# Kernel optimization log

Measured on AMD Instinct MI355X. Metric: run time of the kernel, lower is better.

Reference implementation:

```python
import jax, jax.numpy as jnp
import numpy as np

NUM_LAYERS = 32
NUM_SLOTS = 128
HIDDEN = 4096
T_WRITE = 128   # == NUM_SLOTS so slot_ids form a permutation (deterministic scatter)
T_READ = 8192
EMA_ALPHA = 0.1


def setup_inputs() -> dict:
    key = jax.random.key(0)
    ks = jax.random.split(key, 4)
    values = jax.random.normal(ks[0], (T_WRITE, HIDDEN), jnp.float32)
    queries = jax.random.normal(ks[1], (T_READ, HIDDEN), jnp.float32)
    memory = jax.random.normal(ks[2], (NUM_LAYERS, NUM_SLOTS, HIDDEN), jnp.float32) * 0.02
    gate_w = jax.random.normal(ks[3], (NUM_LAYERS, HIDDEN), jnp.float32) * (1.0 / np.sqrt(HIDDEN))
    gate_b = jnp.zeros((NUM_LAYERS,), jnp.float32)
    return {
        "values": values,
        "queries": queries,
        "memory": memory,
        "gate_w": gate_w,
        "gate_b": gate_b,
        "layer_idx": 0,
        "k": 8,
        "ptr": 0,
    }


def reference(values, queries, memory, gate_w, gate_b, layer_idx, k, ptr):
    # ---- write(): EMA scatter into one layer's slots ----
    mem_l = memory[layer_idx]                                  # [N, d]
    g = jax.nn.sigmoid(values @ gate_w[layer_idx] + gate_b[layer_idx])[:, None]  # [T,1]
    T = values.shape[0]
    slot_ids = (ptr + jnp.arange(T)) % NUM_SLOTS               # [T]
    current = mem_l[slot_ids]                                  # gather [T, d]
    updated = EMA_ALPHA * g * values + (1.0 - EMA_ALPHA) * current
    mem_new = mem_l.at[slot_ids].set(updated)                  # scatter-write [N, d]

    # ---- read(): matmul -> top-k -> gather -> softmax -> weighted sum ----
    scale = 1.0 / jnp.sqrt(jnp.float32(HIDDEN))
    scores = (queries @ mem_new.T) * scale                     # [T_read, N]
    topk_scores, topk_idx = jax.lax.top_k(scores, k)           # [T_read, k]
    attn = jax.nn.softmax(topk_scores, axis=-1)                # [T_read, k]
    topk_v = mem_new[topk_idx]                                 # gather [T_read, k, d]
    out = jnp.einsum('tk,tkd->td', attn, topk_v)               # [T_read, d]
    return out
```

## Files before the change

### kernel.cpp

```cpp
#include <hip/hip_runtime.h>
#include <math.h>

#define D 4096
#define NSLOTS 128
#define TR 8192
#define NKQ 8
#define KCH 512
#define EPS_TRIG 1e-3f
#define WIN 5e-4f

typedef __attribute__((ext_vector_type(8))) short bf16x8;
typedef __attribute__((ext_vector_type(4))) float f32x4;

union BV { bf16x8 v; unsigned u[4]; };

__device__ __forceinline__ unsigned short bfrne(float x) {
  unsigned u = __float_as_uint(x);
  unsigned r = u + 0x7fffu + ((u >> 16) & 1u);
  return (unsigned short)(r >> 16);
}

__device__ __forceinline__ void gload16(const void* gsrc, void* ldst) {
  __builtin_amdgcn_global_load_lds(
      (const __attribute__((address_space(1))) void*)gsrc,
      (__attribute__((address_space(3))) void*)ldst, 16, 0, 0);
}

__global__ __launch_bounds__(256) void update_mem_kernel(
    const float* __restrict__ values, const float* __restrict__ memory,
    const float* __restrict__ gate_w, const float* __restrict__ gate_b,
    const int* __restrict__ layer_idx_p, const int* __restrict__ ptr_p,
    int T_W, float* __restrict__ ws_mem,
    unsigned short* __restrict__ MFh,
    unsigned short* __restrict__ BTFh, unsigned short* __restrict__ BTFm) {
  const int l = layer_idx_p[0], p = ptr_p[0], s = blockIdx.x, tid = threadIdx.x;
  int t0 = ((s - p) % NSLOTS + NSLOTS) % NSLOTS;
  const bool written = (t0 < T_W);
  const int t = written ? (t0 + ((T_W - 1 - t0) / NSLOTS) * NSLOTS) : 0;
  const float* mrow = memory + ((size_t)l * NSLOTS + s) * D;
  const float* vrow = values + (size_t)t * D;

  float acoef = 0.f, bcoef = 1.0f;
  if (written) {
    const float* gw = gate_w + (size_t)l * D;
    double acc = 0.0;
    for (int j = tid; j < D; j += 256)
      acc += (double)vrow[j] * (double)gw[j];
    for (int off = 32; off; off >>= 1) acc += __shfl_down(acc, off, 64);
    __shared__ double wsum[4];
    if ((tid & 63) == 0) wsum[tid >> 6] = acc;
    __syncthreads();
    double dot = wsum[0] + wsum[1] + wsum[2] + wsum[3];
    float x = (float)dot + gate_b[l];
    float g = 1.0f / (1.0f + expf(-x));
    acoef = 0.1f * g; bcoef = 0.9f;
  }

  const int sg = s >> 4, fr_s = s & 15;
  const int ksS = s >> 5, foS = (s >> 3) & 3, posS = s & 7;
  for (int j8 = tid; j8 < D / 8; j8 += 256) {
    float4 mv0 = ((const float4*)mrow)[j8 * 2];
    float4 mv1 = ((const float4*)mrow)[j8 * 2 + 1];
    float4 vv0 = make_float4(0.f, 0.f, 0.f, 0.f), vv1 = vv0;
    if (written) {
      vv0 = ((const float4*)vrow)[j8 * 2];
      vv1 = ((const float4*)vrow)[j8 * 2 + 1];
    }
    float ov[8];
    ov[0] = acoef * vv0.x + bcoef * mv0.x;
    ov[1] = acoef * vv0.y + bcoef * mv0.y;
    ov[2] = acoef * vv0.z + bcoef * mv0.z;
    ov[3] = acoef * vv0.w + bcoef * mv0.w;
    ov[4] = acoef * vv1.x + bcoef * mv1.x;
    ov[5] = acoef * vv1.y + bcoef * mv1.y;
    ov[6] = acoef * vv1.z + bcoef * mv1.z;
    ov[7] = acoef * vv1.w + bcoef * mv1.w;
    ((float4*)(ws_mem + (size_t)s * D))[j8 * 2] =
        make_float4(ov[0], ov[1], ov[2], ov[3]);
    ((float4*)(ws_mem + (size_t)s * D))[j8 * 2 + 1] =
        make_float4(ov[4], ov[5], ov[6], ov[7]);

    unsigned short h[8], md[8];
#pragma unroll
    for (int e = 0; e < 8; ++e) {
      h[e] = bfrne(ov[e]);
      float f = __uint_as_float((unsigned)h[e] << 16);
      md[e] = bfrne(ov[e] - f);
    }
    const int ks = j8 >> 2, fo = j8 & 3;
    const size_t unit = (size_t)ks * 512 + sg * 64 + fo * 16 + fr_s;
    uint4 hp;
    hp.x = (unsigned)h[0] | ((unsigned)h[1] << 16);
    hp.y = (unsigned)h[2] | ((unsigned)h[3] << 16);
    hp.z = (unsigned)h[4] | ((unsigned)h[5] << 16);
    hp.w = (unsigned)h[6] | ((unsigned)h[7] << 16);
    ((uint4*)MFh)[unit] = hp;
#pragma unroll
    for (int e = 0; e < 8; ++e) {
      int c = j8 * 8 + e;
      size_t u = ((size_t)(c >> 4) * 4 + ksS) * 64 + foS * 16 + (c & 15);
      BTFh[u * 8 + posS] = h[e];
      BTFm[u * 8 + posS] = md[e];
    }
  }
}

__global__ __launch_bounds__(256) void scores_kernel(
    const float* __restrict__ queries, const unsigned short* __restrict__ MFh,
    float* __restrict__ part) {
  __shared__ float Qs[2][4096];

  const int tid = threadIdx.x, lane = tid & 63, w = tid >> 6;
  const int fr = lane & 15, fo = lane >> 4;
  const int qt = blockIdx.x >> 3, kq = blockIdx.x & (NKQ - 1);
  const int qbase = qt * 128;
  const int kbase = kq * KCH;

  const int rl = lane >> 3, ul = lane & 7;
  const int su = ul ^ rl;
  const float* qsrc[4];
#pragma unroll
  for (int i = 0; i < 4; ++i) {
    int g = w * 4 + i;
    qsrc[i] = queries + (size_t)(qbase + 8 * g + rl) * D + kbase + su * 4;
  }

  const unsigned short* bh_base = MFh + (size_t)lane * 8;
  const size_t kqoff = (size_t)kq * 16 * 512 * 8;

  f32x4 acc[2][8];
#pragma unroll
  for (int rg = 0; rg < 2; ++rg)
#pragma unroll
    for (int cg = 0; cg < 8; ++cg) acc[rg][cg] = (f32x4){0.f, 0.f, 0.f, 0.f};

#define STG(B, S) do {                                                       \
    const int k0_ = (S) * 32;                                                \
    _Pragma("unroll")                                                        \
    for (int i = 0; i < 4; ++i)                                              \
      gload16(qsrc[i] + k0_, &Qs[B][(w * 4 + i) * 256]);                     \
  } while (0)

#define CMP(B, S) do {                                                       \
    const size_t soff = kqoff + (size_t)(S) * 512 * 8;                       \
    bf16x8 bh_[8];                                                           \
    _Pragma("unroll")                                                        \
    for (int cg = 0; cg < 8; ++cg)                                           \
      bh_[cg] = *(const bf16x8*)(bh_base + soff + cg * 64 * 8);              \
    _Pragma("unroll")                                                        \
    for (int rg = 0; rg < 2; ++rg) {                                         \
      const int row = w * 32 + rg * 16 + fr;                                 \
      float4 a0 = *(const float4*)&Qs[B][row * 32 + (((fo * 2) ^ (row & 7)) << 2)]; \
      float4 a1 = *(const float4*)&Qs[B][row * 32 + ((((fo * 2) | 1) ^ (row & 7)) << 2)]; \
      float qf[8] = {a0.x, a0.y, a0.z, a0.w, a1.x, a1.y, a1.z, a1.w};        \
      BV ah;                                                                 \
      _Pragma("unroll")                                                      \
      for (int i = 0; i < 4; ++i) {                                          \
        unsigned u0 = __float_as_uint(qf[2 * i]);                            \
        unsigned u1 = __float_as_uint(qf[2 * i + 1]);                        \
        ah.u[i] = (u0 >> 16) | (u1 & 0xffff0000u);         \
      }                                                                      \
      _Pragma("unroll")                                                      \
      for (int cg = 0; cg < 8; ++cg)                                         \
        acc[rg][cg] = __builtin_amdgcn_mfma_f32_16x16x32_bf16(ah.v, bh_[cg], acc[rg][cg], 0, 0, 0); \
    }                                                                        \
  } while (0)

  STG(0, 0);
  __syncthreads();
  for (int s = 0; s < 16; ++s) {
    const int cur = s & 1;
    if (s < 15) STG(cur ^ 1, s + 1);
    CMP(cur, s);
    __syncthreads();
  }
#undef STG
#undef CMP

  float* op = part + ((size_t)kq * TR + qbase) * NSLOTS;
#pragma unroll
  for (int rg = 0; rg < 2; ++rg)
#pragma unroll
    for (int cg = 0; cg < 8; ++cg)
#pragma unroll
      for (int r = 0; r < 4; ++r)
        op[(size_t)(w * 32 + rg * 16 + fo * 4 + r) * NSLOTS + cg * 16 + fr] =
            acc[rg][cg][r];
}

__device__ __forceinline__ unsigned mapf(float f) {
  unsigned u = __float_as_uint(f);
  return (u & 0x80000000u) ? ~u : (u | 0x80000000u);
}
__device__ __forceinline__ float unmapf(unsigned u) {
  return __uint_as_float((u & 0x80000000u) ? (u & 0x7fffffffu) : ~u);
}

__device__ __forceinline__ void wave_select(
    float va, float vb, int l, int k, int iters,
    float &m, float &sum, bool &sela, bool &selb, float &vkm1, float &vkk) {
  m = 0.f; sum = 0.f; sela = false; selb = false; vkm1 = 0.f; vkk = -3.4e38f;
  for (int it = 0; it < iters; ++it) {
    unsigned long long ka =
        ((unsigned long long)mapf(va) << 32) | (unsigned)(127 - l);
    unsigned long long kb =
        ((unsigned long long)mapf(vb) << 32) | (unsigned)(63 - l);
    unsigned long long key = ka > kb ? ka : kb;
#pragma unroll
    for (int off = 32; off; off >>= 1) {
      unsigned long long o = __shfl_xor(key, off, 64);
      if (o > key) key = o;
    }
    int idx = 127 - (int)(unsigned)(key & 0xffffffffULL);
    float val = unmapf((unsigned)(key >> 32));
    if (it == 0) m = val;
    if (it < k) sum += expf(val - m);
    if (it == k - 1) vkm1 = val;
    if (it == k) vkk = val;
    if (idx == l) { sela = sela || (it < k); va = -INFINITY; }
    if (idx == l + 64) { selb = selb || (it < k); vb = -INFINITY; }
  }
}

__device__ __forceinline__ float rescore_slot(const float* __restrict__ qrow,
                                              const float* __restrict__ mrow,
                                              int l) {
  double acc = 0.0;
#pragma unroll 4
  for (int c = 0; c < 16; ++c) {
    int j = c * 256 + l * 4;
    float4 qv = *(const float4*)(qrow + j);
    float4 mv = *(const float4*)(mrow + j);
    acc += (double)qv.x * (double)mv.x;
    acc += (double)qv.y * (double)mv.y;
    acc += (double)qv.z * (double)mv.z;
    acc += (double)qv.w * (double)mv.w;
  }
#pragma unroll
  for (int off = 32; off; off >>= 1) acc += __shfl_xor(acc, off, 64);
  return (float)(acc * 0.015625);
}

__global__ __launch_bounds__(256) void topk_kernel(
    const float* __restrict__ part, const float* __restrict__ ws_mem,
    const float* __restrict__ queries, const int* __restrict__ k_p,
    unsigned short* __restrict__ AFh, unsigned short* __restrict__ AFm) {
  const int w = threadIdx.x >> 6, l = threadIdx.x & 63;
  const int row = blockIdx.x * 4 + w;
  int k = k_p[0];
  if (k < 1) k = 1;
  if (k > NSLOTS) k = NSLOTS;
  const int ksel = (k < NSLOTS) ? k + 1 : k;

  float origa = 0.f, origb = 0.f;
#pragma unroll
  for (int kq = 0; kq < NKQ; ++kq) {
    origa += part[((size_t)kq * TR + row) * NSLOTS + l];
    origb += part[((size_t)kq * TR + row) * NSLOTS + 64 + l];
  }
  origa *= 0.015625f;
  origb *= 0.015625f;

  float m, sum, vkm1, vkk;
  bool sela, selb;
  wave_select(origa, origb, l, k, ksel, m, sum, sela, selb, vkm1, vkk);

  if (ksel > k && (vkm1 - vkk) < EPS_TRIG) {
    const float* qrow = queries + (size_t)row * D;
    float lo = vkk - WIN, hi = vkm1 + WIN;
    unsigned long long ba = __ballot(origa >= lo && origa <= hi);
    unsigned long long bb = __ballot(origb >= lo && origb <= hi);
    while (ba) {
      int s = __ffsll(ba) - 1; ba &= ba - 1;
      float ex = rescore_slot(qrow, ws_mem + (size_t)s * D, l);
      if (l == s) origa = ex;
    }
    while (bb) {
      int s = __ffsll(bb) - 1; bb &= bb - 1;
      float ex = rescore_slot(qrow, ws_mem + (size_t)(s + 64) * D, l);
      if (l == s) origb = ex;
    }
    wave_select(origa, origb, l, k, k, m, sum, sela, selb, vkm1, vkk);
  }

  const float inv = 1.0f / sum;
  float wa = sela ? expf(origa - m) * inv : 0.f;
  float wb = selb ? expf(origb - m) * inv : 0.f;

  unsigned short ha = bfrne(wa);
  unsigned short ma = bfrne(wa - __uint_as_float((unsigned)ha << 16));
  unsigned short hb = bfrne(wb);
  unsigned short mb = bfrne(wb - __uint_as_float((unsigned)hb << 16));

  const int rg = row >> 4, frr = row & 15;
  const size_t ua =
      (((size_t)rg * 4 + (l >> 5)) * 64 + ((l >> 3) & 3) * 16 + frr) * 8 + (l & 7);
  const size_t ub =
      (((size_t)rg * 4 + (l >> 5) + 2) * 64 + ((l >> 3) & 3) * 16 + frr) * 8 + (l & 7);
  AFh[ua] = ha; AFm[ua] = ma;
  AFh[ub] = hb; AFm[ub] = mb;
}

__global__ __launch_bounds__(256) void gather_kernel(
    const unsigned short* __restrict__ AFh, const unsigned short* __restrict__ AFm,
    const unsigned short* __restrict__ BTFh, const unsigned short* __restrict__ BTFm,
    float* __restrict__ out) {
  const int tid = threadIdx.x, lane = tid & 63, w = tid >> 6;
  const int fr = lane & 15, fo = lane >> 4;
  const int rowblk = blockIdx.x >> 5, colblk = blockIdx.x & 31;
  const int r0 = rowblk * 128 + w * 32;
  const int rg0 = r0 >> 4;

  bf16x8 a_h[2][4], a_m[2][4];
#pragma unroll
  for (int rg = 0; rg < 2; ++rg)
#pragma unroll
    for (int ks = 0; ks < 4; ++ks) {
      const size_t u = (((size_t)(rg0 + rg) * 4 + ks) * 64 + lane) * 8;
      a_h[rg][ks] = *(const bf16x8*)(AFh + u);
      a_m[rg][ks] = *(const bf16x8*)(AFm + u);
    }

#pragma unroll 2
  for (int cgi = 0; cgi < 8; ++cgi) {
    const int cg = colblk * 8 + cgi;
    bf16x8 b_h[4], b_m[4];
#pragma unroll
    for (int ks = 0; ks < 4; ++ks) {
      const size_t u = (((size_t)cg * 4 + ks) * 64 + lane) * 8;
      b_h[ks] = *(const bf16x8*)(BTFh + u);
      b_m[ks] = *(const bf16x8*)(BTFm + u);
    }
    const int col = cg * 16 + fr;
#pragma unroll
    for (int rg = 0; rg < 2; ++rg) {
      f32x4 acc = {0.f, 0.f, 0.f, 0.f};
#pragma unroll
      for (int ks = 0; ks < 4; ++ks) {
        acc = __builtin_amdgcn_mfma_f32_16x16x32_bf16(a_m[rg][ks], b_h[ks], acc, 0, 0, 0);
        acc = __builtin_amdgcn_mfma_f32_16x16x32_bf16(a_h[rg][ks], b_m[ks], acc, 0, 0, 0);
        acc = __builtin_amdgcn_mfma_f32_16x16x32_bf16(a_h[rg][ks], b_h[ks], acc, 0, 0, 0);
      }
#pragma unroll
      for (int r = 0; r < 4; ++r)
        out[(size_t)(r0 + rg * 16 + fo * 4 + r) * D + col] = acc[r];
    }
  }
}

extern "C" void kernel_launch(void* const* d_in, const int* in_sizes, int n_in,
                              void* d_out, int out_size, void* d_ws, size_t ws_size,
                              hipStream_t stream) {
  const float* values  = (const float*)d_in[0];
  const float* queries = (const float*)d_in[1];
  const float* memory  = (const float*)d_in[2];
  const float* gate_w  = (const float*)d_in[3];
  const float* gate_b  = (const float*)d_in[4];
  const int* layer_idx = (const int*)d_in[5];
  const int* k_p       = (const int*)d_in[6];
  const int* ptr_p     = (const int*)d_in[7];

  const int T_W = in_sizes[0] / D;
  const int T_R = in_sizes[1] / D;

  float* ws_mem = (float*)d_ws;
  float* part   = ws_mem + (size_t)NSLOTS * D;
  unsigned short* MFh  = (unsigned short*)(part + (size_t)NKQ * TR * NSLOTS);
  unsigned short* BTFh = MFh  + (size_t)NSLOTS * D;
  unsigned short* BTFm = BTFh + (size_t)NSLOTS * D;
  unsigned short* AFh  = BTFm + (size_t)NSLOTS * D;
  unsigned short* AFm  = AFh  + (size_t)T_R * NSLOTS;

  update_mem_kernel<<<NSLOTS, 256, 0, stream>>>(
      values, memory, gate_w, gate_b, layer_idx, ptr_p, T_W,
      ws_mem, MFh, BTFh, BTFm);
  scores_kernel<<<(T_R / 128) * NKQ, 256, 0, stream>>>(queries, MFh, part);
  topk_kernel<<<T_R / 4, 256, 0, stream>>>(part, ws_mem, queries, k_p, AFh, AFm);
  gather_kernel<<<(T_R / 128) * (D / 128), 256, 0, stream>>>(AFh, AFm, BTFh, BTFm,
                                                             (float*)d_out);
}
```

Before: 132.8 us.

## Deepen query staging to four LDS buffers with explicit vmcnt waits

The scores kernel now stages query tiles into a four-deep ring of LDS buffers, issuing loads two steps ahead instead of one. It replaces the per-iteration __syncthreads with an explicit s_waitcnt on outstanding vector loads plus a single s_barrier, and fully unrolls the K loop. The goal is to hide global-load latency behind the MFMA work and cut synchronisation stalls. In exchange the kernel uses twice the shared memory (64 KB), which may reduce occupancy. Correctness now depends on the hand-written vmcnt counts matching the order in which loads are issued.

```diff
diff --git a/kernel.cpp b/kernel.cpp
--- a/kernel.cpp
+++ b/kernel.cpp
@@ -108,7 +108,7 @@
 __global__ __launch_bounds__(256) void scores_kernel(
     const float* __restrict__ queries, const unsigned short* __restrict__ MFh,
     float* __restrict__ part) {
-  __shared__ float Qs[2][4096];
+  __shared__ float Qs[4][4096];
 
   const int tid = threadIdx.x, lane = tid & 63, w = tid >> 6;
   const int fr = lane & 15, fo = lane >> 4;
@@ -121,12 +121,10 @@
   const float* qsrc[4];
 #pragma unroll
   for (int i = 0; i < 4; ++i) {
-    int g = w * 4 + i;
-    qsrc[i] = queries + (size_t)(qbase + 8 * g + rl) * D + kbase + su * 4;
-  }
-
-  const unsigned short* bh_base = MFh + (size_t)lane * 8;
-  const size_t kqoff = (size_t)kq * 16 * 512 * 8;
+    int dl = w * 4 + i;
+    qsrc[i] = queries + (size_t)(qbase + 8 * dl + rl) * D + kbase + su * 4;
+  }
+  const unsigned short* bsrc = MFh + (size_t)kq * 16 * 4096 + (size_t)lane * 8;
 
   f32x4 acc[2][8];
 #pragma unroll
@@ -134,48 +132,46 @@
 #pragma unroll
     for (int cg = 0; cg < 8; ++cg) acc[rg][cg] = (f32x4){0.f, 0.f, 0.f, 0.f};
 
-#define STG(B, S) do {                                                       \
-    const int k0_ = (S) * 32;                                                \
+  const int rowA = w * 32 + fr;
+
+#define STGQ(B_, S_) do {                                                    \
     _Pragma("unroll")                                                        \
     for (int i = 0; i < 4; ++i)                                              \
-      gload16(qsrc[i] + k0_, &Qs[B][(w * 4 + i) * 256]);                     \
+      gload16(qsrc[i] + (S_) * 32, &Qs[B_][(w * 4 + i) * 256]);              \
   } while (0)
 
-#define CMP(B, S) do {                                                       \
-    const size_t soff = kqoff + (size_t)(S) * 512 * 8;                       \
-    bf16x8 bh_[8];                                                           \
-    _Pragma("unroll")                                                        \
-    for (int cg = 0; cg < 8; ++cg)                                           \
-      bh_[cg] = *(const bf16x8*)(bh_base + soff + cg * 64 * 8);              \
-    _Pragma("unroll")                                                        \
-    for (int rg = 0; rg < 2; ++rg) {                                         \
-      const int row = w * 32 + rg * 16 + fr;                                 \
-      float4 a0 = *(const float4*)&Qs[B][row * 32 + (((fo * 2) ^ (row & 7)) << 2)]; \
-      float4 a1 = *(const float4*)&Qs[B][row * 32 + ((((fo * 2) | 1) ^ (row & 7)) << 2)]; \
-      float qf[8] = {a0.x, a0.y, a0.z, a0.w, a1.x, a1.y, a1.z, a1.w};        \
-      BV ah;                                                                 \
-      _Pragma("unroll")                                                      \
-      for (int i = 0; i < 4; ++i) {                                          \
-        unsigned u0 = __float_as_uint(qf[2 * i]);                            \
-        unsigned u1 = __float_as_uint(qf[2 * i + 1]);                        \
-        ah.u[i] = (u0 >> 16) | (u1 & 0xffff0000u);         \
-      }                                                                      \
-      _Pragma("unroll")                                                      \
-      for (int cg = 0; cg < 8; ++cg)                                         \
-        acc[rg][cg] = __builtin_amdgcn_mfma_f32_16x16x32_bf16(ah.v, bh_[cg], acc[rg][cg], 0, 0, 0); \
-    }                                                                        \
-  } while (0)
-
-  STG(0, 0);
-  __syncthreads();
+  STGQ(0, 0);
+  STGQ(1, 1);
+#pragma unroll
   for (int s = 0; s < 16; ++s) {
-    const int cur = s & 1;
-    if (s < 15) STG(cur ^ 1, s + 1);
-    CMP(cur, s);
-    __syncthreads();
-  }
-#undef STG
-#undef CMP
+    bf16x8 bh_[8];
+#pragma unroll
+    for (int cg = 0; cg < 8; ++cg)
+      bh_[cg] = *(const bf16x8*)(bsrc + (size_t)s * 4096 + cg * 64 * 8);
+    if (s + 2 < 16) STGQ((s + 2) & 3, s + 2);
+    if (s <= 13) asm volatile("s_waitcnt vmcnt(4)" ::: "memory");
+    else         asm volatile("s_waitcnt vmcnt(0)" ::: "memory");
+    __builtin_amdgcn_sched_barrier(0);
+    __builtin_amdgcn_s_barrier();
+#pragma unroll
+    for (int rg = 0; rg < 2; ++rg) {
+      const int row = rowA + rg * 16;
+      float4 a0 = *(const float4*)&Qs[s & 3][row * 32 + (((fo * 2) ^ (row & 7)) << 2)];
+      float4 a1 = *(const float4*)&Qs[s & 3][row * 32 + ((((fo * 2) | 1) ^ (row & 7)) << 2)];
+      float qf[8] = {a0.x, a0.y, a0.z, a0.w, a1.x, a1.y, a1.z, a1.w};
+      BV ah;
+#pragma unroll
+      for (int i = 0; i < 4; ++i) {
+        unsigned u0 = __float_as_uint(qf[2 * i]);
+        unsigned u1 = __float_as_uint(qf[2 * i + 1]);
+        ah.u[i] = (u0 >> 16) | (u1 & 0xffff0000u);
+      }
+#pragma unroll
+      for (int cg = 0; cg < 8; ++cg)
+        acc[rg][cg] = __builtin_amdgcn_mfma_f32_16x16x32_bf16(ah.v, bh_[cg], acc[rg][cg], 0, 0, 0);
+    }
+  }
+#undef STGQ
 
   float* op = part + ((size_t)kq * TR + qbase) * NSLOTS;
 #pragma unroll
```

New measurement: 133.1 us. No clear change (+0.2%).
